# Kernel tuning notes

Hardware: AMD Instinct MI355X
Metric: run time of the kernel (lower is better)

Reference implementation:

```python
import jax, jax.numpy as jnp
import numpy as np

KERNEL_CONST = 2.5652997311834374e-21  # constant value filling the depthwise kernel


def setup_inputs() -> dict:
    key = jax.random.key(0)
    H = W = 1024   # arg0_1, arg1_1: output (= input) spatial size
    Kh = Kw = 1024  # arg3_1, arg4_1: kernel spatial size (full-image box kernel)
    x = jax.random.normal(key, (2, 3, H, W), dtype=jnp.float32)
    return {"arg0_1": H, "arg1_1": W, "arg2_1": x, "arg3_1": Kh, "arg4_1": Kw}


def _box_conv(x, H, W, Kh, Kw):
    # reflection pad exactly as the torch graph: left/top = (k-1)//2, right/bottom = k-1-left
    pl = (Kw - 1) // 2
    pr = (Kw - 1) - pl
    pt = (Kh - 1) // 2
    pb = (Kh - 1) - pt
    p = jnp.pad(x, ((0, 0), (0, 0), (pt, pb), (pl, pr)), mode="reflect")
    # depthwise conv with a constant-valued [Kh,Kw] kernel == const * sliding box sum.
    # Computed in O(HW) via an integral image (2D prefix sum) instead of dense conv.
    S = jnp.cumsum(jnp.cumsum(p, axis=-2), axis=-1)
    S = jnp.pad(S, ((0, 0), (0, 0), (1, 0), (1, 0)))  # zero row/col for inclusive sums
    box = (S[..., Kh:Kh + H, Kw:Kw + W]
           - S[..., :H, Kw:Kw + W]
           - S[..., Kh:Kh + H, :W]
           + S[..., :H, :W])
    return jnp.float32(KERNEL_CONST) * box  # shape [2, 3, H, W]


def reference(arg0_1, arg1_1, arg2_1, arg3_1, arg4_1):
    return _box_conv(arg2_1, arg0_1, arg1_1, arg3_1, arg4_1)
```

## Files before the change

kernel.cpp:

```cpp
#include <hip/hip_runtime.h>


static constexpr float KC = 2.5652997311834374e-21f;
#define IMG (1024 * 1024)

__device__ __forceinline__ float hwindow(const float* S, int o) {
    float r = 0.f;
    if (o <= 510) r += S[512 - o] - S[1];
    const int b0 = o > 511 ? o - 511 : 0;
    const int b1 = o + 513 < 1024 ? o + 513 : 1024;
    r += S[b1] - S[b0];
    if (o >= 512) r += S[1023] - S[1534 - o];
    return r;
}

__device__ __forceinline__ void hrow_emit2(float4 u0, float4 u1,
                                           float* S0, float* S1,
                                           float* wt0, float* wt1,
                                           float* orow0, float* orow1, int t) {
    const float a0 = u0.x, a1 = a0 + u0.y, a2 = a1 + u0.z, a3 = a2 + u0.w;
    const float b0 = u1.x, b1 = b0 + u1.y, b2 = b1 + u1.z, b3 = b2 + u1.w;
    const int lane = t & 63, wave = t >> 6;
    float incA = a3, incB = b3;
    #pragma unroll
    for (int off = 1; off < 64; off <<= 1) {
        float nA = __shfl_up(incA, off);
        float nB = __shfl_up(incB, off);
        if (lane >= off) { incA += nA; incB += nB; }
    }
    if (lane == 63) { wt0[wave] = incA; wt1[wave] = incB; }
    __syncthreads();
    float woffA = 0.f, woffB = 0.f;
    for (int w = 0; w < wave; ++w) { woffA += wt0[w]; woffB += wt1[w]; }
    const float exA = woffA + incA - a3;
    const float exB = woffB + incB - b3;
    S0[4 * t + 0] = exA;      S1[4 * t + 0] = exB;
    S0[4 * t + 1] = exA + a0; S1[4 * t + 1] = exB + b0;
    S0[4 * t + 2] = exA + a1; S1[4 * t + 2] = exB + b1;
    S0[4 * t + 3] = exA + a2; S1[4 * t + 3] = exB + b2;
    if (t == 255) { S0[1024] = exA + a3; S1[1024] = exB + b3; }
    __syncthreads();
    const int ox = 4 * t;
    float4 o0, o1;
    o0.x = KC * hwindow(S0, ox + 0);
    o0.y = KC * hwindow(S0, ox + 1);
    o0.z = KC * hwindow(S0, ox + 2);
    o0.w = KC * hwindow(S0, ox + 3);
    o1.x = KC * hwindow(S1, ox + 0);
    o1.y = KC * hwindow(S1, ox + 1);
    o1.z = KC * hwindow(S1, ox + 2);
    o1.w = KC * hwindow(S1, ox + 3);
    reinterpret_cast<float4*>(orow0)[t] = o0;
    reinterpret_cast<float4*>(orow1)[t] = o1;
}

__global__ __launch_bounds__(256) void scanx_kernel(const float* __restrict__ x,
                                                    float* __restrict__ BP) {
    __shared__ float B[257][33];
    const int t = threadIdx.x;
    const int ch = blockIdx.x >> 5, cg = blockIdx.x & 31;
    const int col0 = cg * 32;
    const int c = t & 31, g = t >> 5;
    const float* xc = x + (size_t)ch * IMG + col0 + c;

    #pragma unroll 4
    for (int i = 0; i < 32; ++i) {
        const int band = g + 8 * i;
        const float* p = xc + (size_t)band * 4 * 1024;
        B[band][c] = (p[0] + p[1024]) + (p[2048] + p[3072]);
    }
    __syncthreads();

    const int lane = t & 63, wv = t >> 6;
    #pragma unroll
    for (int i = 0; i < 8; ++i) {
        const int cc = wv * 8 + i;
        float v0 = B[lane][cc], v1 = B[lane + 64][cc],
              v2 = B[lane + 128][cc], v3 = B[lane + 192][cc];
        float i0 = v0, i1 = v1, i2 = v2, i3 = v3;
        #pragma unroll
        for (int off = 1; off < 64; off <<= 1) {
            float n0 = __shfl_up(i0, off), n1 = __shfl_up(i1, off);
            float n2 = __shfl_up(i2, off), n3 = __shfl_up(i3, off);
            if (lane >= off) { i0 += n0; i1 += n1; i2 += n2; i3 += n3; }
        }
        const float t0 = __shfl(i0, 63), t1 = __shfl(i1, 63), t2 = __shfl(i2, 63);
        B[lane][cc]       = i0 - v0;
        B[lane + 64][cc]  = t0 + i1 - v1;
        B[lane + 128][cc] = t0 + t1 + i2 - v2;
        B[lane + 192][cc] = t0 + t1 + t2 + i3 - v3;
        if (lane == 63) B[256][cc] = t0 + t1 + t2 + i3;
    }
    __syncthreads();

    float* Bp = BP + (size_t)ch * 257 * 1024 + col0;
    #pragma unroll
    for (int i = 0; i < 33; ++i) {
        const int idx = i * 256 + t;
        if (idx < 257 * 32) {
            const int k = idx >> 5, cw = idx & 31;
            Bp[(size_t)k * 1024 + cw] = B[k][cw];
        }
    }
}

__global__ __launch_bounds__(256) void vslideh_kernel(const float* __restrict__ x,
                                                      const float* __restrict__ BP,
                                                      float* __restrict__ out) {
    __shared__ float S[2][1025];
    __shared__ float wtot[2][4];
    const int t = threadIdx.x;
    const int ch = blockIdx.x >> 8, band = blockIdx.x & 255;
    const int O = band * 4;
    const float* xc = x + (size_t)ch * IMG;
    const float* Bc = BP + (size_t)ch * 257 * 1024;
    float* oc = out + (size_t)ch * IMG;

    #define LD4(base, row) (reinterpret_cast<const float4*>((base) + (size_t)(row) * 1024)[t])

    float4 u0, u1, u2, u3;
    if (band < 128) {
        const float4 bA = LD4(Bc, (512 - O) >> 2);
        const float4 x0 = LD4(xc, 0);
        const float4 bB = LD4(Bc, (512 + O) >> 2);
        const float4 xb = LD4(xc, O + 512);
        u0.x = bA.x - x0.x + bB.x + xb.x;
        u0.y = bA.y - x0.y + bB.y + xb.y;
        u0.z = bA.z - x0.z + bB.z + xb.z;
        u0.w = bA.w - x0.w + bB.w + xb.w;
        {
            const float4 a = LD4(xc, O + 513), s = LD4(xc, 511 - O);
            u1.x = u0.x + a.x - s.x; u1.y = u0.y + a.y - s.y;
            u1.z = u0.z + a.z - s.z; u1.w = u0.w + a.w - s.w;
        }
        {
            const float4 a = LD4(xc, O + 514), s = LD4(xc, 510 - O);
            u2.x = u1.x + a.x - s.x; u2.y = u1.y + a.y - s.y;
            u2.z = u1.z + a.z - s.z; u2.w = u1.w + a.w - s.w;
        }
        if (band == 127) {
            u3 = LD4(Bc, 256);
        } else {
            const float4 a = LD4(xc, O + 515), s = LD4(xc, 509 - O);
            u3.x = u2.x + a.x - s.x; u3.y = u2.y + a.y - s.y;
            u3.z = u2.z + a.z - s.z; u3.w = u2.w + a.w - s.w;
        }
    } else {
        const float4 bt = LD4(Bc, 256);
        const float4 bA = LD4(Bc, (O - 512) >> 2);
        const float4 xm = LD4(xc, 1023);
        const float4 bB = LD4(Bc, (1536 - O) >> 2);
        const float4 xf = LD4(xc, 1535 - O);
        float4 acc;
        acc.x = bt.x - bA.x + (bt.x - xm.x) - (bB.x - xf.x);
        acc.y = bt.y - bA.y + (bt.y - xm.y) - (bB.y - xf.y);
        acc.z = bt.z - bA.z + (bt.z - xm.z) - (bB.z - xf.z);
        acc.w = bt.w - bA.w + (bt.w - xm.w) - (bB.w - xf.w);
        {
            const float4 a = LD4(xc, 1534 - O), s = LD4(xc, O - 512);
            u0.x = acc.x + a.x - s.x; u0.y = acc.y + a.y - s.y;
            u0.z = acc.z + a.z - s.z; u0.w = acc.w + a.w - s.w;
        }
        {
            const float4 a = LD4(xc, 1533 - O), s = LD4(xc, O - 511);
            u1.x = u0.x + a.x - s.x; u1.y = u0.y + a.y - s.y;
            u1.z = u0.z + a.z - s.z; u1.w = u0.w + a.w - s.w;
        }
        {
            const float4 a = LD4(xc, 1532 - O), s = LD4(xc, O - 510);
            u2.x = u1.x + a.x - s.x; u2.y = u1.y + a.y - s.y;
            u2.z = u1.z + a.z - s.z; u2.w = u1.w + a.w - s.w;
        }
        {
            const float4 a = LD4(xc, 1531 - O), s = LD4(xc, O - 509);
            u3.x = u2.x + a.x - s.x; u3.y = u2.y + a.y - s.y;
            u3.z = u2.z + a.z - s.z; u3.w = u2.w + a.w - s.w;
        }
    }
    #undef LD4

    hrow_emit2(u0, u1, S[0], S[1], wtot[0], wtot[1],
               oc + (size_t)O * 1024, oc + (size_t)(O + 1) * 1024, t);
    hrow_emit2(u2, u3, S[0], S[1], wtot[0], wtot[1],
               oc + (size_t)(O + 2) * 1024, oc + (size_t)(O + 3) * 1024, t);
}

extern "C" void kernel_launch(void* const* d_in, const int* in_sizes, int n_in,
                              void* d_out, int out_size, void* d_ws, size_t ws_size,
                              hipStream_t stream) {
    const float* x = (const float*)d_in[2];
    float* out = (float*)d_out;
    float* BP = (float*)d_ws;
    scanx_kernel<<<192, 256, 0, stream>>>(x, BP);
    vslideh_kernel<<<1536, 256, 0, stream>>>(x, BP, out);
}
```

Before: 30.77 us.

## Pair mirrored row bands per block to share reflected input row loads

Each block of the vertical-slide kernel now handles both band i in the top half and its mirror band near the bottom. Under reflection padding both bands read the same input rows and prefix rows, so one set of loads serves both. The grid is halved to 768 blocks of 8 output rows each, which removes the top/bottom branch and cuts redundant global reads. In exchange each block carries more registers and a longer serial chain of scans and syncs, with fewer blocks left to hide latency.

```diff
diff --git a/kernel.cpp b/kernel.cpp
--- a/kernel.cpp
+++ b/kernel.cpp
@@ -110,79 +110,71 @@
     __shared__ float S[2][1025];
     __shared__ float wtot[2][4];
     const int t = threadIdx.x;
-    const int ch = blockIdx.x >> 8, band = blockIdx.x & 255;
-    const int O = band * 4;
+    const int ch = blockIdx.x >> 7, i = blockIdx.x & 127;
+    const int O = 4 * i;
+    const int Oh = 1020 - O;
     const float* xc = x + (size_t)ch * IMG;
     const float* Bc = BP + (size_t)ch * 257 * 1024;
     float* oc = out + (size_t)ch * IMG;
 
     #define LD4(base, row) (reinterpret_cast<const float4*>((base) + (size_t)(row) * 1024)[t])
 
+    const float4 x0 = LD4(xc, 0);
+    const float4 xm = LD4(xc, 1023);
+    const float4 a0 = LD4(xc, O + 511);
+    const float4 a1 = LD4(xc, O + 512);
+    const float4 a2 = LD4(xc, O + 513);
+    const float4 a3 = LD4(xc, O + 514);
+    const float4 a4 = LD4(xc, O + 515);
+    const float4 sA = LD4(xc, 511 - O);
+    const float4 sB = LD4(xc, 510 - O);
+    const float4 sC = LD4(xc, 509 - O);
+    const float4 sD = LD4(xc, 508 - O);
+    const float4 bLA = LD4(Bc, 128 - i);
+    const float4 bLB = LD4(Bc, 128 + i);
+    const float4 bHA = LD4(Bc, 127 - i);
+    const float4 bHB = LD4(Bc, 129 + i);
+    const float4 bT  = LD4(Bc, 256);
+    #undef LD4
+
     float4 u0, u1, u2, u3;
-    if (band < 128) {
-        const float4 bA = LD4(Bc, (512 - O) >> 2);
-        const float4 x0 = LD4(xc, 0);
-        const float4 bB = LD4(Bc, (512 + O) >> 2);
-        const float4 xb = LD4(xc, O + 512);
-        u0.x = bA.x - x0.x + bB.x + xb.x;
-        u0.y = bA.y - x0.y + bB.y + xb.y;
-        u0.z = bA.z - x0.z + bB.z + xb.z;
-        u0.w = bA.w - x0.w + bB.w + xb.w;
-        {
-            const float4 a = LD4(xc, O + 513), s = LD4(xc, 511 - O);
-            u1.x = u0.x + a.x - s.x; u1.y = u0.y + a.y - s.y;
-            u1.z = u0.z + a.z - s.z; u1.w = u0.w + a.w - s.w;
-        }
-        {
-            const float4 a = LD4(xc, O + 514), s = LD4(xc, 510 - O);
-            u2.x = u1.x + a.x - s.x; u2.y = u1.y + a.y - s.y;
-            u2.z = u1.z + a.z - s.z; u2.w = u1.w + a.w - s.w;
-        }
-        if (band == 127) {
-            u3 = LD4(Bc, 256);
-        } else {
-            const float4 a = LD4(xc, O + 515), s = LD4(xc, 509 - O);
-            u3.x = u2.x + a.x - s.x; u3.y = u2.y + a.y - s.y;
-            u3.z = u2.z + a.z - s.z; u3.w = u2.w + a.w - s.w;
-        }
+    u0.x = bLA.x - x0.x + bLB.x + a1.x;
+    u0.y = bLA.y - x0.y + bLB.y + a1.y;
+    u0.z = bLA.z - x0.z + bLB.z + a1.z;
+    u0.w = bLA.w - x0.w + bLB.w + a1.w;
+    u1.x = u0.x + a2.x - sA.x; u1.y = u0.y + a2.y - sA.y;
+    u1.z = u0.z + a2.z - sA.z; u1.w = u0.w + a2.w - sA.w;
+    u2.x = u1.x + a3.x - sB.x; u2.y = u1.y + a3.y - sB.y;
+    u2.z = u1.z + a3.z - sB.z; u2.w = u1.w + a3.w - sB.w;
+    if (i == 127) {
+        u3 = bT;
     } else {
-        const float4 bt = LD4(Bc, 256);
-        const float4 bA = LD4(Bc, (O - 512) >> 2);
-        const float4 xm = LD4(xc, 1023);
-        const float4 bB = LD4(Bc, (1536 - O) >> 2);
-        const float4 xf = LD4(xc, 1535 - O);
-        float4 acc;
-        acc.x = bt.x - bA.x + (bt.x - xm.x) - (bB.x - xf.x);
-        acc.y = bt.y - bA.y + (bt.y - xm.y) - (bB.y - xf.y);
-        acc.z = bt.z - bA.z + (bt.z - xm.z) - (bB.z - xf.z);
-        acc.w = bt.w - bA.w + (bt.w - xm.w) - (bB.w - xf.w);
-        {
-            const float4 a = LD4(xc, 1534 - O), s = LD4(xc, O - 512);
-            u0.x = acc.x + a.x - s.x; u0.y = acc.y + a.y - s.y;
-            u0.z = acc.z + a.z - s.z; u0.w = acc.w + a.w - s.w;
-        }
-        {
-            const float4 a = LD4(xc, 1533 - O), s = LD4(xc, O - 511);
-            u1.x = u0.x + a.x - s.x; u1.y = u0.y + a.y - s.y;
-            u1.z = u0.z + a.z - s.z; u1.w = u0.w + a.w - s.w;
-        }
-        {
-            const float4 a = LD4(xc, 1532 - O), s = LD4(xc, O - 510);
-            u2.x = u1.x + a.x - s.x; u2.y = u1.y + a.y - s.y;
-            u2.z = u1.z + a.z - s.z; u2.w = u1.w + a.w - s.w;
-        }
-        {
-            const float4 a = LD4(xc, 1531 - O), s = LD4(xc, O - 509);
-            u3.x = u2.x + a.x - s.x; u3.y = u2.y + a.y - s.y;
-            u3.z = u2.z + a.z - s.z; u3.w = u2.w + a.w - s.w;
-        }
+        u3.x = u2.x + a4.x - sC.x; u3.y = u2.y + a4.y - sC.y;
+        u3.z = u2.z + a4.z - sC.z; u3.w = u2.w + a4.w - sC.w;
     }
-    #undef LD4
+
+    float4 acc, v0, v1, v2, v3;
+    acc.x = bT.x - bHA.x + (bT.x - xm.x) - (bHB.x - a4.x);
+    acc.y = bT.y - bHA.y + (bT.y - xm.y) - (bHB.y - a4.y);
+    acc.z = bT.z - bHA.z + (bT.z - xm.z) - (bHB.z - a4.z);
+    acc.w = bT.w - bHA.w + (bT.w - xm.w) - (bHB.w - a4.w);
+    v0.x = acc.x + a3.x - sD.x; v0.y = acc.y + a3.y - sD.y;
+    v0.z = acc.z + a3.z - sD.z; v0.w = acc.w + a3.w - sD.w;
+    v1.x = v0.x + a2.x - sC.x; v1.y = v0.y + a2.y - sC.y;
+    v1.z = v0.z + a2.z - sC.z; v1.w = v0.w + a2.w - sC.w;
+    v2.x = v1.x + a1.x - sB.x; v2.y = v1.y + a1.y - sB.y;
+    v2.z = v1.z + a1.z - sB.z; v2.w = v1.w + a1.w - sB.w;
+    v3.x = v2.x + a0.x - sA.x; v3.y = v2.y + a0.y - sA.y;
+    v3.z = v2.z + a0.z - sA.z; v3.w = v2.w + a0.w - sA.w;
 
     hrow_emit2(u0, u1, S[0], S[1], wtot[0], wtot[1],
                oc + (size_t)O * 1024, oc + (size_t)(O + 1) * 1024, t);
     hrow_emit2(u2, u3, S[0], S[1], wtot[0], wtot[1],
                oc + (size_t)(O + 2) * 1024, oc + (size_t)(O + 3) * 1024, t);
+    hrow_emit2(v0, v1, S[0], S[1], wtot[0], wtot[1],
+               oc + (size_t)Oh * 1024, oc + (size_t)(Oh + 1) * 1024, t);
+    hrow_emit2(v2, v3, S[0], S[1], wtot[0], wtot[1],
+               oc + (size_t)(Oh + 2) * 1024, oc + (size_t)(Oh + 3) * 1024, t);
 }
 
 extern "C" void kernel_launch(void* const* d_in, const int* in_sizes, int n_in,
@@ -192,5 +184,5 @@
     float* out = (float*)d_out;
     float* BP = (float*)d_ws;
     scanx_kernel<<<192, 256, 0, stream>>>(x, BP);
-    vslideh_kernel<<<1536, 256, 0, stream>>>(x, BP, out);
+    vslideh_kernel<<<768, 256, 0, stream>>>(x, BP, out);
 }
```

Result: no change. 31.13 us (+1.2%).
